# Kernel tuning notes

Measured on AMD Instinct MI355X. Metric: run time of the kernel, lower is better.

Reference implementation:

```python
import jax, jax.numpy as jnp
import numpy as np

N_NODES = 100000
N_EDGES = 1600000
N_GRAPHS = 5000
IN_DIM = 14   # 11 QM9 node features + 3 pos coords
HID = 256


def setup_inputs() -> dict:
    key = jax.random.key(0)
    ks = jax.random.split(key, 12)
    x = jax.random.normal(ks[0], (N_NODES, 11), dtype=jnp.float32)
    pos = jax.random.normal(ks[1], (N_NODES, 3), dtype=jnp.float32)
    edge_index = jax.random.randint(ks[2], (2, N_EDGES), 0, N_NODES, dtype=jnp.int32)
    batch = jnp.sort(jax.random.randint(ks[3], (N_NODES,), 0, N_GRAPHS, dtype=jnp.int32))
    # SAGEConv params (PyG default: lin_l on mean-aggregated neighbors w/ bias, lin_r on root no bias)
    s1 = 1.0 / np.sqrt(IN_DIM)
    s2 = 1.0 / np.sqrt(HID)
    W1l = jax.random.uniform(ks[4], (IN_DIM, HID), jnp.float32, -s1, s1)
    b1 = jax.random.uniform(ks[5], (HID,), jnp.float32, -s1, s1)
    W1r = jax.random.uniform(ks[6], (IN_DIM, HID), jnp.float32, -s1, s1)
    W2l = jax.random.uniform(ks[7], (HID, HID), jnp.float32, -s2, s2)
    b2 = jax.random.uniform(ks[8], (HID,), jnp.float32, -s2, s2)
    W2r = jax.random.uniform(ks[9], (HID, HID), jnp.float32, -s2, s2)
    Wout = jax.random.uniform(ks[10], (HID, 1), jnp.float32, -s2, s2)
    bout = jax.random.uniform(ks[11], (1,), jnp.float32, -s2, s2)
    return {"x": x, "pos": pos, "edge_index": edge_index, "batch": batch,
            "W1l": W1l, "b1": b1, "W1r": W1r,
            "W2l": W2l, "b2": b2, "W2r": W2r,
            "Wout": Wout, "bout": bout}


def _sage_conv(h, src, dst, Wl, bl, Wr):
    # mean aggregation of source node features into destination nodes
    msg = h[src]                                              # [E, D]
    agg = jax.ops.segment_sum(msg, dst, num_segments=N_NODES)  # [N, D]
    cnt = jax.ops.segment_sum(jnp.ones((src.shape[0],), h.dtype), dst,
                              num_segments=N_NODES)
    mean = agg / jnp.maximum(cnt, 1.0)[:, None]
    return mean @ Wl + bl + h @ Wr


def reference(x, pos, edge_index, batch, W1l, b1, W1r, W2l, b2, W2r, Wout, bout):
    src, dst = edge_index[0], edge_index[1]
    h = jnp.concatenate([x, pos], axis=1)                     # [N, 14]
    h = jax.nn.relu(_sage_conv(h, src, dst, W1l, b1, W1r))    # [N, HID]
    h = jax.nn.relu(_sage_conv(h, src, dst, W2l, b2, W2r))    # [N, HID]
    # global mean pool over graphs
    gsum = jax.ops.segment_sum(h, batch, num_segments=N_GRAPHS)  # [G, HID]
    gcnt = jax.ops.segment_sum(jnp.ones((h.shape[0],), h.dtype), batch,
                               num_segments=N_GRAPHS)
    g = gsum / jnp.maximum(gcnt, 1.0)[:, None]
    return g @ Wout + bout                                    # [G, 1]
```

## Files before the change

### kernel.cpp

```cpp
#include <hip/hip_runtime.h>

#define N_N 100000
#define N_E 1600000
#define N_G 5000
#define HID 256
#define IND 14

#define NBUK 391
#define CAP 5120
#define CH3 8192
#define NFB 196

typedef __bf16 bf16x8 __attribute__((ext_vector_type(8)));
typedef float f32x4 __attribute__((ext_vector_type(4)));
typedef unsigned short u16;
typedef unsigned int u32;

constexpr size_t OFF_OUTS  = 0;
constexpr size_t OFF_GCUR  = 5120;
constexpr size_t ZERO_END  = 11520;
constexpr size_t ZERO_BYTES = ZERO_END * 4;
constexpr size_t OFF_GCNT  = 11520;
constexpr size_t OFF_ROWP  = 16640;
constexpr size_t OFF_DEG   = 116736;
constexpr size_t OFF_EBUF  = 216832;
constexpr size_t OFF_CSRC  = 2218752;
constexpr size_t OFF_H1B   = 4220672;
constexpr size_t OFF_WCAT  = 17032960;
constexpr size_t OFF_XP    = 17098496;
constexpr size_t OFF_MEAN1B= 17898496;
constexpr size_t OFF_W1CAT = 30710784;

__device__ __forceinline__ u32 f2b(float f) {
    u32 u = __float_as_uint(f);
    u32 r = u + 0x7FFFu + ((u >> 16) & 1u);
    return r >> 16;
}

#define ADD8(acc, v) do { \
    acc[0] += __uint_as_float(v.x << 16); \
    acc[1] += __uint_as_float(v.x & 0xFFFF0000u); \
    acc[2] += __uint_as_float(v.y << 16); \
    acc[3] += __uint_as_float(v.y & 0xFFFF0000u); \
    acc[4] += __uint_as_float(v.z << 16); \
    acc[5] += __uint_as_float(v.z & 0xFFFF0000u); \
    acc[6] += __uint_as_float(v.w << 16); \
    acc[7] += __uint_as_float(v.w & 0xFFFF0000u); \
} while (0)

#define PACK_N (N_N * 16)
#define WCAT_N (256 * 512)
#define W1CAT_N (256 * 32)
#define PREP_TOT (PACK_N + WCAT_N + W1CAT_N + N_G)
#define PREP_BLKS ((PREP_TOT + 511) / 512)
__global__ __launch_bounds__(512) void k_bfill_prep(const int* __restrict__ ei, int* __restrict__ gcur,
                                                    u32* __restrict__ ebuf,
                                                    const float* __restrict__ x, const float* __restrict__ pos,
                                                    const int* __restrict__ batch,
                                                    const float* __restrict__ W2l, const float* __restrict__ W2r,
                                                    const float* __restrict__ W1l, const float* __restrict__ W1r,
                                                    u16* __restrict__ xpb, float* __restrict__ gcnt,
                                                    u16* __restrict__ wcat, u16* __restrict__ w1cat) {
    __shared__ int hist[NBUK];
    __shared__ int lcur[NBUK];
    __shared__ int gbase[NBUK];
    __shared__ int wsum[8];
    __shared__ u32 stage[CH3];
    __shared__ u16 bstage[CH3];
    int t = threadIdx.x;
    if (blockIdx.x >= NFB) {
        int idx = (blockIdx.x - NFB) * 512 + t;
        if (idx < PACK_N) {
            int n = idx >> 4, f = idx & 15;
            float v = 0.f;
            if (f < 11) v = x[n * 11 + f];
            else if (f < 14) v = pos[n * 3 + (f - 11)];
            xpb[idx] = (u16)f2b(v);
        } else if (idx < PACK_N + WCAT_N) {
            int i2 = idx - PACK_N;
            int n = i2 >> 9, k = i2 & 511;
            float v = (k < 256) ? W2l[k * HID + n] : W2r[(k - 256) * HID + n];
            wcat[(size_t)n * 512 + k] = (u16)f2b(v);
        } else if (idx < PACK_N + WCAT_N + W1CAT_N) {
            int i2 = idx - PACK_N - WCAT_N;
            int n = i2 >> 5, k = i2 & 31;
            float v = 0.f;
            if (k < IND) v = W1l[k * HID + n];
            else if (k >= 16 && k < 16 + IND) v = W1r[(k - 16) * HID + n];
            w1cat[(size_t)n * 32 + k] = (u16)f2b(v);
        } else if (idx < PREP_TOT) {
            int g = idx - PACK_N - WCAT_N - W1CAT_N;
            int lo = 0, hi = N_N;
            while (lo < hi) { int mid = (lo + hi) >> 1; if (batch[mid] < g) lo = mid + 1; else hi = mid; }
            int lo2 = lo, hi2 = N_N;
            while (lo2 < hi2) { int mid = (lo2 + hi2) >> 1; if (batch[mid] < g + 1) lo2 = mid + 1; else hi2 = mid; }
            gcnt[g] = (float)(lo2 - lo);
        }
        return;
    }
    int lane = t & 63, wv = t >> 6;
    int base = blockIdx.x * CH3;
    for (int i = t; i < NBUK; i += 512) hist[i] = 0;
    __syncthreads();
#pragma unroll
    for (int i = 0; i < 16; i++) {
        int e = base + i * 512 + t;
        if (e < N_E) atomicAdd(&hist[ei[N_E + e] >> 8], 1);
    }
    __syncthreads();
    int v = (t < NBUK) ? hist[t] : 0;
    int inc = v;
#pragma unroll
    for (int off = 1; off < 64; off <<= 1) {
        int u = __shfl_up(inc, off, 64);
        if (lane >= off) inc += u;
    }
    if (lane == 63) wsum[wv] = inc;
    __syncthreads();
    int pre = 0;
    for (int i = 0; i < wv; i++) pre += wsum[i];
    int inclusive = inc + pre;
    int excl = inclusive - v;
    if (t < NBUK) lcur[t] = excl;
    int blockcnt = 0;
#pragma unroll
    for (int i = 0; i < 8; i++) blockcnt += wsum[i];
    __syncthreads();
#pragma unroll
    for (int i = 0; i < 16; i++) {
        int e = base + i * 512 + t;
        if (e < N_E) {
            int d = ei[N_E + e];
            int s = ei[e];
            int b = d >> 8;
            int p = atomicAdd(&lcur[b], 1);
            stage[p] = (u32)s | ((u32)(d & 255) << 17);
            bstage[p] = (u16)b;
        }
    }
    __syncthreads();
    if (t < NBUK) {
        int c = hist[t];
        int o = c ? atomicAdd(&gcur[t * 16], c) : 0;
        gbase[t] = t * CAP + o - excl;
    }
    __syncthreads();
#pragma unroll
    for (int i = 0; i < 16; i++) {
        int p = i * 512 + t;
        if (p < blockcnt) {
            int b = bstage[p];
            ebuf[gbase[b] + p] = stage[p];
        }
    }
}

__global__ __launch_bounds__(256) void k_sort(const u32* __restrict__ ebuf, const int* __restrict__ gcur,
                                              int* __restrict__ csrc, int* __restrict__ deg,
                                              int* __restrict__ rowp) {
    __shared__ int degL[256];
    __shared__ int curL[256];
    __shared__ int wsum[4];
    int t = threadIdx.x;
    int lane = t & 63, wv = t >> 6;
    int b = blockIdx.x;
    int bs = b * CAP;
    int be = bs + gcur[b * 16];
    degL[t] = 0;
    __syncthreads();
    for (int e = bs + t; e < be; e += 256)
        atomicAdd(&degL[ebuf[e] >> 17], 1);
    __syncthreads();
    int myDeg = degL[t];
    int inc = myDeg;
#pragma unroll
    for (int off = 1; off < 64; off <<= 1) {
        int u = __shfl_up(inc, off, 64);
        if (lane >= off) inc += u;
    }
    if (lane == 63) wsum[wv] = inc;
    __syncthreads();
    int pre = 0;
    for (int i = 0; i < wv; i++) pre += wsum[i];
    int excl = inc + pre - myDeg;
    int node = (b << 8) + t;
    deg[node] = myDeg;
    rowp[node] = bs + excl;
    curL[t] = bs + excl;
    __syncthreads();
    for (int e = bs + t; e < be; e += 256) {
        u32 w = ebuf[e];
        int p = atomicAdd(&curL[w >> 17], 1);
        csrc[p] = (int)(w & 0x1FFFFu);
    }
}

__global__ __launch_bounds__(256) void k_layer1(const u16* __restrict__ xpb,
                                                const int* __restrict__ rowp, const int* __restrict__ deg,
                                                const int* __restrict__ csrc,
                                                const u16* __restrict__ w1cat, const float* __restrict__ b1,
                                                u16* __restrict__ h1b) {
    __shared__ u16 As[16][32];
    __shared__ u16 outS[16][256];
    int tid = threadIdx.x;
    int wave = tid >> 6, lane = tid & 63;
    int fp = lane & 7;
    int eg = lane >> 3;
#pragma unroll
    for (int nn = 0; nn < 4; nn++) {
        int s = wave * 4 + nn;
        int node = blockIdx.x * 16 + s;
        int st = rowp[node], dg = deg[node];
        int end = st + dg;
        float a0 = 0.f, a1 = 0.f, b0 = 0.f, b1v = 0.f;
        int e = st + eg;
        for (; e + 8 < end; e += 16) {
            int nb1 = csrc[e];
            int nb2 = csrc[e + 8];
            u32 v1 = *(const u32*)(xpb + (size_t)nb1 * 16 + fp * 2);
            u32 v2 = *(const u32*)(xpb + (size_t)nb2 * 16 + fp * 2);
            a0 += __uint_as_float(v1 << 16);
            a1 += __uint_as_float(v1 & 0xFFFF0000u);
            b0 += __uint_as_float(v2 << 16);
            b1v += __uint_as_float(v2 & 0xFFFF0000u);
        }
        if (e < end) {
            int nb = csrc[e];
            u32 v = *(const u32*)(xpb + (size_t)nb * 16 + fp * 2);
            a0 += __uint_as_float(v << 16);
            a1 += __uint_as_float(v & 0xFFFF0000u);
        }
        a0 += b0; a1 += b1v;
        if (eg == 1) {
            *(u32*)&As[s][16 + fp * 2] = *(const u32*)(xpb + (size_t)node * 16 + fp * 2);
        }
#pragma unroll
        for (int off = 32; off >= 8; off >>= 1) {
            a0 += __shfl_down(a0, off);
            a1 += __shfl_down(a1, off);
        }
        if (eg == 0) {
            float inv = 1.f / (float)max(dg, 1);
            *(u32*)&As[s][fp * 2] = f2b(a0 * inv) | (f2b(a1 * inv) << 16);
        }
    }
    __syncthreads();
    int quad = lane >> 4, m16 = lane & 15;
    bf16x8 afrag = *(const bf16x8*)&As[m16][quad * 8];
#pragma unroll
    for (int u = 0; u < 4; u++) {
        int feat = wave * 64 + u * 16 + m16;
        bf16x8 bfrag = *(const bf16x8*)(w1cat + (size_t)feat * 32 + quad * 8);
        f32x4 d = {0.f, 0.f, 0.f, 0.f};
        d = __builtin_amdgcn_mfma_f32_16x16x32_bf16(afrag, bfrag, d, 0, 0, 0);
        float bj = b1[feat];
#pragma unroll
        for (int i = 0; i < 4; i++) {
            int row = quad * 4 + i;
            outS[row][feat] = (u16)f2b(fmaxf(d[i] + bj, 0.f));
        }
    }
    __syncthreads();
    int r = tid >> 4, c = tid & 15;
    uint4* dst = (uint4*)(h1b + ((size_t)(blockIdx.x * 16 + r)) * HID + c * 16);
    dst[0] = *(const uint4*)&outS[r][c * 16];
    dst[1] = *(const uint4*)&outS[r][c * 16 + 8];
}

__global__ __launch_bounds__(256) void k_agg(const u16* __restrict__ h1b, const int* __restrict__ rowp,
                                             const int* __restrict__ deg, const int* __restrict__ csrc,
                                             u16* __restrict__ mean1b) {
    int tid = threadIdx.x;
    int node = blockIdx.x * 4 + (tid >> 6);
    int lane = tid & 63;
    int half = lane >> 5, l32 = lane & 31;
    int st = rowp[node], dg = deg[node];
    int end = st + dg;
    const size_t roff = (size_t)l32 * 8;
    float accA[8] = {}, accB[8] = {};
    int e = st + half;
    for (; e + 2 < end; e += 4) {
        int nb1 = csrc[e];
        int nb2 = csrc[e + 2];
        uint4 v1 = *(const uint4*)(h1b + (size_t)nb1 * HID + roff);
        uint4 v2 = *(const uint4*)(h1b + (size_t)nb2 * HID + roff);
        ADD8(accA, v1);
        ADD8(accB, v2);
    }
    if (e < end) {
        int nb = csrc[e];
        uint4 v = *(const uint4*)(h1b + (size_t)nb * HID + roff);
        ADD8(accA, v);
    }
    float acc[8];
#pragma unroll
    for (int j = 0; j < 8; j++) acc[j] = accA[j] + accB[j];
#pragma unroll
    for (int j = 0; j < 8; j++) acc[j] += __shfl_down(acc[j], 32);
    if (lane < 32) {
        float inv = 1.f / (float)max(dg, 1);
        uint4 o;
        o.x = f2b(acc[0] * inv) | (f2b(acc[1] * inv) << 16);
        o.y = f2b(acc[2] * inv) | (f2b(acc[3] * inv) << 16);
        o.z = f2b(acc[4] * inv) | (f2b(acc[5] * inv) << 16);
        o.w = f2b(acc[6] * inv) | (f2b(acc[7] * inv) << 16);
        *(uint4*)(mean1b + (size_t)node * HID + roff) = o;
    }
}

__global__ __launch_bounds__(256, 2) void k_layer2(const u16* __restrict__ mean1b, const u16* __restrict__ h1b,
                                                   const u16* __restrict__ wcat, const float* __restrict__ b2,
                                                   const int* __restrict__ batch, const float* __restrict__ Wout,
                                                   float* __restrict__ outsum) {
    __shared__ u16 Bs[2][256][40];
    int tid = threadIdx.x;
    int wave = tid >> 6, lane = tid & 63;
    int quad = lane >> 4, m16 = lane & 15;
    int bm = blockIdx.x;
    const size_t r0 = (size_t)(bm * 128 + wave * 32 + m16) * HID + quad * 8;
    const size_t r1 = r0 + 16 * HID;
    f32x4 acc[2][16] = {};
    uint4 a0 = *(const uint4*)(mean1b + r0);
    uint4 a1 = *(const uint4*)(mean1b + r1);
    for (int kt2 = 0; kt2 < 8; kt2++) {
        __syncthreads();
#pragma unroll
        for (int h = 0; h < 2; h++) {
            int kt = kt2 * 2 + h;
#pragma unroll
            for (int i = 0; i < 4; i++) {
                int cidx = tid + 256 * i;
                int n = cidx >> 2, kc = cidx & 3;
                *(uint4*)&Bs[h][n][kc * 8] =
                    *(const uint4*)(wcat + (size_t)n * 512 + kt * 32 + kc * 8);
            }
        }
        __syncthreads();
#pragma unroll
        for (int h = 0; h < 2; h++) {
            int kt = kt2 * 2 + h;
            uint4 cur0 = a0, cur1 = a1;
            if (kt < 15) {
                int kg = (kt + 1) * 32;
                const u16* An = (kg < 256) ? (mean1b + kg) : (h1b + (kg - 256));
                a0 = *(const uint4*)(An + r0);
                a1 = *(const uint4*)(An + r1);
            }
            bf16x8 af0 = __builtin_bit_cast(bf16x8, cur0);
            bf16x8 af1 = __builtin_bit_cast(bf16x8, cur1);
#pragma unroll
            for (int u = 0; u < 16; u++) {
                bf16x8 bf = *(const bf16x8*)&Bs[h][u * 16 + m16][quad * 8];
                acc[0][u] = __builtin_amdgcn_mfma_f32_16x16x32_bf16(af0, bf, acc[0][u], 0, 0, 0);
                acc[1][u] = __builtin_amdgcn_mfma_f32_16x16x32_bf16(af1, bf, acc[1][u], 0, 0, 0);
            }
        }
    }
    float wo[16], bb[16];
#pragma unroll
    for (int u = 0; u < 16; u++) { int col = u * 16 + m16; wo[u] = Wout[col]; bb[u] = b2[col]; }
#pragma unroll
    for (int t = 0; t < 2; t++) {
#pragma unroll
        for (int i = 0; i < 4; i++) {
            float p = 0.f;
#pragma unroll
            for (int u = 0; u < 16; u++)
                p = fmaf(fmaxf(acc[t][u][i] + bb[u], 0.f), wo[u], p);
#pragma unroll
            for (int off = 8; off > 0; off >>= 1) p += __shfl_down(p, off, 16);
            int row = bm * 128 + wave * 32 + t * 16 + quad * 4 + i;
            if (m16 == 0 && row < N_N) atomicAdd(&outsum[batch[row]], p);
        }
    }
}

__global__ __launch_bounds__(256) void k_out(const float* __restrict__ outsum, const float* __restrict__ gcnt,
                                             const float* __restrict__ bout, float* __restrict__ out) {
    int g = blockIdx.x * 256 + threadIdx.x;
    if (g < N_G) out[g] = outsum[g] / fmaxf(gcnt[g], 1.f) + bout[0];
}

extern "C" void kernel_launch(void* const* d_in, const int* in_sizes, int n_in,
                              void* d_out, int out_size, void* d_ws, size_t ws_size,
                              hipStream_t stream) {
    const float* x    = (const float*)d_in[0];
    const float* pos  = (const float*)d_in[1];
    const int*   ei   = (const int*)d_in[2];
    const int*   batch= (const int*)d_in[3];
    const float* W1l  = (const float*)d_in[4];
    const float* b1   = (const float*)d_in[5];
    const float* W1r  = (const float*)d_in[6];
    const float* W2l  = (const float*)d_in[7];
    const float* b2   = (const float*)d_in[8];
    const float* W2r  = (const float*)d_in[9];
    const float* Wout = (const float*)d_in[10];
    const float* bout = (const float*)d_in[11];
    float* out = (float*)d_out;
    float* ws  = (float*)d_ws;

    float* outs  = ws + OFF_OUTS;
    int*   gcur  = (int*)(ws + OFF_GCUR);
    float* gcnt  = ws + OFF_GCNT;
    int*   rowp  = (int*)(ws + OFF_ROWP);
    int*   deg   = (int*)(ws + OFF_DEG);
    u32*   ebuf  = (u32*)(ws + OFF_EBUF);
    int*   csrc  = (int*)(ws + OFF_CSRC);
    u16*   h1b   = (u16*)(ws + OFF_H1B);
    u16*   wcat  = (u16*)(ws + OFF_WCAT);
    u16*   xpb   = (u16*)(ws + OFF_XP);
    u16*   mean1b= (u16*)(ws + OFF_MEAN1B);
    u16*   w1cat = (u16*)(ws + OFF_W1CAT);

    hipMemsetAsync(d_ws, 0, ZERO_BYTES, stream);
    k_bfill_prep<<<NFB + PREP_BLKS, 512, 0, stream>>>(
        ei, gcur, ebuf, x, pos, batch, W2l, W2r, W1l, W1r, xpb, gcnt, wcat, w1cat);
    k_sort  <<<NBUK, 256, 0, stream>>>(ebuf, gcur, csrc, deg, rowp);
    k_layer1<<<N_N / 16, 256, 0, stream>>>(xpb, rowp, deg, csrc, w1cat, b1, h1b);
    k_agg   <<<N_N / 4, 256, 0, stream>>>(h1b, rowp, deg, csrc, mean1b);
    k_layer2<<<(N_N + 127) / 128, 256, 0, stream>>>(mean1b, h1b, wcat, b2, batch, Wout, outs);
    k_out   <<<(N_G + 255) / 256, 256, 0, stream>>>(outs, gcnt, bout, out);
}
```

Measured before the change: 325.0 us.

## Recompute layer-1 outputs per edge from compact 32-wide inputs instead of gathering h1

Layer 1 now also writes each node's 32-wide bf16 input row (mean-aggregated features plus root features) into a scratch buffer that reuses the edge buffer. The second aggregation no longer gathers 256-wide h1 rows per neighbor. It gathers the 32-wide rows and recomputes relu(z·W1+b1) per edge with MFMA, masking padded lanes, then averages. This replaces 512-byte gathers with 64-byte gathers at the cost of redundant matrix math per edge, about 16 MFMAs per 16 edges per wave.

```diff
diff --git a/kernel.cpp b/kernel.cpp
--- a/kernel.cpp
+++ b/kernel.cpp
@@ -199,7 +199,7 @@
                                                 const int* __restrict__ rowp, const int* __restrict__ deg,
                                                 const int* __restrict__ csrc,
                                                 const u16* __restrict__ w1cat, const float* __restrict__ b1,
-                                                u16* __restrict__ h1b) {
+                                                u16* __restrict__ h1b, u16* __restrict__ zb) {
     __shared__ u16 As[16][32];
     __shared__ u16 outS[16][256];
     int tid = threadIdx.x;
@@ -245,6 +245,10 @@
         }
     }
     __syncthreads();
+    {
+        int s = tid >> 4, kp = tid & 15;
+        *(u32*)(zb + (size_t)(blockIdx.x * 16 + s) * 32 + kp * 2) = *(const u32*)&As[s][kp * 2];
+    }
     int quad = lane >> 4, m16 = lane & 15;
     bf16x8 afrag = *(const bf16x8*)&As[m16][quad * 8];
 #pragma unroll
@@ -267,45 +271,53 @@
     dst[1] = *(const uint4*)&outS[r][c * 16 + 8];
 }
 
-__global__ __launch_bounds__(256) void k_agg(const u16* __restrict__ h1b, const int* __restrict__ rowp,
+__global__ __launch_bounds__(256) void k_agg(const u16* __restrict__ zb, const int* __restrict__ rowp,
                                              const int* __restrict__ deg, const int* __restrict__ csrc,
+                                             const u16* __restrict__ w1cat, const float* __restrict__ b1,
                                              u16* __restrict__ mean1b) {
+    __shared__ u16 outW[4][256];
     int tid = threadIdx.x;
-    int node = blockIdx.x * 4 + (tid >> 6);
-    int lane = tid & 63;
-    int half = lane >> 5, l32 = lane & 31;
+    int wv = tid >> 6, lane = tid & 63;
+    int quad = lane >> 4, m16 = lane & 15;
+    int node = blockIdx.x * 4 + wv;
     int st = rowp[node], dg = deg[node];
     int end = st + dg;
-    const size_t roff = (size_t)l32 * 8;
-    float accA[8] = {}, accB[8] = {};
-    int e = st + half;
-    for (; e + 2 < end; e += 4) {
-        int nb1 = csrc[e];
-        int nb2 = csrc[e + 2];
-        uint4 v1 = *(const uint4*)(h1b + (size_t)nb1 * HID + roff);
-        uint4 v2 = *(const uint4*)(h1b + (size_t)nb2 * HID + roff);
-        ADD8(accA, v1);
-        ADD8(accB, v2);
-    }
-    if (e < end) {
-        int nb = csrc[e];
-        uint4 v = *(const uint4*)(h1b + (size_t)nb * HID + roff);
-        ADD8(accA, v);
-    }
-    float acc[8];
-#pragma unroll
-    for (int j = 0; j < 8; j++) acc[j] = accA[j] + accB[j];
-#pragma unroll
-    for (int j = 0; j < 8; j++) acc[j] += __shfl_down(acc[j], 32);
-    if (lane < 32) {
-        float inv = 1.f / (float)max(dg, 1);
-        uint4 o;
-        o.x = f2b(acc[0] * inv) | (f2b(acc[1] * inv) << 16);
-        o.y = f2b(acc[2] * inv) | (f2b(acc[3] * inv) << 16);
-        o.z = f2b(acc[4] * inv) | (f2b(acc[5] * inv) << 16);
-        o.w = f2b(acc[6] * inv) | (f2b(acc[7] * inv) << 16);
-        *(uint4*)(mean1b + (size_t)node * HID + roff) = o;
-    }
+
+    bf16x8 bfrag[16];
+    float bb[16];
+#pragma unroll
+    for (int u = 0; u < 16; u++) {
+        bfrag[u] = *(const bf16x8*)(w1cat + (size_t)(u * 16 + m16) * 32 + quad * 8);
+        bb[u] = b1[u * 16 + m16];
+    }
+    float acc[16] = {};
+    for (int cb = 0; cb < dg; cb += 16) {
+        int e = st + cb + m16;
+        int nb = (e < end) ? csrc[e] : csrc[st];
+        bf16x8 afrag = *(const bf16x8*)(zb + (size_t)nb * 32 + quad * 8);
+        float mk[4];
+#pragma unroll
+        for (int i = 0; i < 4; i++)
+            mk[i] = (cb + quad * 4 + i < dg) ? 1.f : 0.f;
+#pragma unroll
+        for (int u = 0; u < 16; u++) {
+            f32x4 d = {0.f, 0.f, 0.f, 0.f};
+            d = __builtin_amdgcn_mfma_f32_16x16x32_bf16(afrag, bfrag[u], d, 0, 0, 0);
+#pragma unroll
+            for (int i = 0; i < 4; i++)
+                acc[u] = fmaf(mk[i], fmaxf(d[i] + bb[u], 0.f), acc[u]);
+        }
+    }
+    float inv = 1.f / (float)max(dg, 1);
+#pragma unroll
+    for (int u = 0; u < 16; u++) {
+        float a = acc[u];
+        a += __shfl_down(a, 32);
+        a += __shfl_down(a, 16);
+        if (quad == 0) outW[wv][u * 16 + m16] = (u16)f2b(a * inv);
+    }
+    if (lane < 32)
+        *(uint4*)(mean1b + (size_t)node * HID + (size_t)lane * 8) = *(const uint4*)&outW[wv][lane * 8];
 }
 
 __global__ __launch_bounds__(256, 2) void k_layer2(const u16* __restrict__ mean1b, const u16* __restrict__ h1b,
@@ -411,13 +423,14 @@
     u16*   xpb   = (u16*)(ws + OFF_XP);
     u16*   mean1b= (u16*)(ws + OFF_MEAN1B);
     u16*   w1cat = (u16*)(ws + OFF_W1CAT);
+    u16*   zb    = (u16*)ebuf;
 
     hipMemsetAsync(d_ws, 0, ZERO_BYTES, stream);
     k_bfill_prep<<<NFB + PREP_BLKS, 512, 0, stream>>>(
         ei, gcur, ebuf, x, pos, batch, W2l, W2r, W1l, W1r, xpb, gcnt, wcat, w1cat);
     k_sort  <<<NBUK, 256, 0, stream>>>(ebuf, gcur, csrc, deg, rowp);
-    k_layer1<<<N_N / 16, 256, 0, stream>>>(xpb, rowp, deg, csrc, w1cat, b1, h1b);
-    k_agg   <<<N_N / 4, 256, 0, stream>>>(h1b, rowp, deg, csrc, mean1b);
+    k_layer1<<<N_N / 16, 256, 0, stream>>>(xpb, rowp, deg, csrc, w1cat, b1, h1b, zb);
+    k_agg   <<<N_N / 4, 256, 0, stream>>>(zb, rowp, deg, csrc, w1cat, b1, mean1b);
     k_layer2<<<(N_N + 127) / 128, 256, 0, stream>>>(mean1b, h1b, wcat, b2, batch, Wout, outs);
     k_out   <<<(N_G + 255) / 256, 256, 0, stream>>>(outs, gcnt, bout, out);
 }
```

Result: slower. 659.7 us (+103.0%).

## Split neighbor aggregation into feature-slice passes for cache locality

Applied to the files above, without the earlier changes.

Restructures the mean-aggregation kernel so the grid is split into 16 passes, each covering a 16-feature slice of every node. Each node is handled by two threads, one per 8-feature half, and the cross-lane shuffle reduction is removed. Each pass's gather working set (a 32-byte slice per node) is small enough to stay cache-resident, which is meant to cut random-gather traffic to HBM. The cost is that the CSR index arrays are re-read in every pass, each thread issues narrow 16-byte scattered loads, and padding to 782×128 nodes means the last block reads past the end of the rowp and deg arrays.

```diff
diff --git a/kernel.cpp b/kernel.cpp
--- a/kernel.cpp
+++ b/kernel.cpp
@@ -267,45 +267,45 @@
     dst[1] = *(const uint4*)&outS[r][c * 16 + 8];
 }
 
+#define NPASS 16
+#define AGG_BPP 782
 __global__ __launch_bounds__(256) void k_agg(const u16* __restrict__ h1b, const int* __restrict__ rowp,
                                              const int* __restrict__ deg, const int* __restrict__ csrc,
                                              u16* __restrict__ mean1b) {
     int tid = threadIdx.x;
-    int node = blockIdx.x * 4 + (tid >> 6);
-    int lane = tid & 63;
-    int half = lane >> 5, l32 = lane & 31;
+    int pass = blockIdx.x / AGG_BPP;
+    int blk  = blockIdx.x % AGG_BPP;
+    int node = blk * 128 + (tid >> 1);
+    int fh = tid & 1;
     int st = rowp[node], dg = deg[node];
     int end = st + dg;
-    const size_t roff = (size_t)l32 * 8;
+    const u16* src = h1b + (size_t)pass * 16 + (size_t)fh * 8;
     float accA[8] = {}, accB[8] = {};
-    int e = st + half;
-    for (; e + 2 < end; e += 4) {
+    int e = st;
+    for (; e + 1 < end; e += 2) {
         int nb1 = csrc[e];
-        int nb2 = csrc[e + 2];
-        uint4 v1 = *(const uint4*)(h1b + (size_t)nb1 * HID + roff);
-        uint4 v2 = *(const uint4*)(h1b + (size_t)nb2 * HID + roff);
+        int nb2 = csrc[e + 1];
+        uint4 v1 = *(const uint4*)(src + (size_t)nb1 * HID);
+        uint4 v2 = *(const uint4*)(src + (size_t)nb2 * HID);
         ADD8(accA, v1);
         ADD8(accB, v2);
     }
     if (e < end) {
         int nb = csrc[e];
-        uint4 v = *(const uint4*)(h1b + (size_t)nb * HID + roff);
+        uint4 v = *(const uint4*)(src + (size_t)nb * HID);
         ADD8(accA, v);
     }
-    float acc[8];
-#pragma unroll
-    for (int j = 0; j < 8; j++) acc[j] = accA[j] + accB[j];
-#pragma unroll
-    for (int j = 0; j < 8; j++) acc[j] += __shfl_down(acc[j], 32);
-    if (lane < 32) {
-        float inv = 1.f / (float)max(dg, 1);
-        uint4 o;
-        o.x = f2b(acc[0] * inv) | (f2b(acc[1] * inv) << 16);
-        o.y = f2b(acc[2] * inv) | (f2b(acc[3] * inv) << 16);
-        o.z = f2b(acc[4] * inv) | (f2b(acc[5] * inv) << 16);
-        o.w = f2b(acc[6] * inv) | (f2b(acc[7] * inv) << 16);
-        *(uint4*)(mean1b + (size_t)node * HID + roff) = o;
-    }
+    float inv = 1.f / (float)max(dg, 1);
+    float a0 = (accA[0] + accB[0]) * inv, a1 = (accA[1] + accB[1]) * inv;
+    float a2 = (accA[2] + accB[2]) * inv, a3 = (accA[3] + accB[3]) * inv;
+    float a4 = (accA[4] + accB[4]) * inv, a5 = (accA[5] + accB[5]) * inv;
+    float a6 = (accA[6] + accB[6]) * inv, a7 = (accA[7] + accB[7]) * inv;
+    uint4 o;
+    o.x = f2b(a0) | (f2b(a1) << 16);
+    o.y = f2b(a2) | (f2b(a3) << 16);
+    o.z = f2b(a4) | (f2b(a5) << 16);
+    o.w = f2b(a6) | (f2b(a7) << 16);
+    *(uint4*)(mean1b + (size_t)node * HID + (size_t)pass * 16 + (size_t)fh * 8) = o;
 }
 
 __global__ __launch_bounds__(256, 2) void k_layer2(const u16* __restrict__ mean1b, const u16* __restrict__ h1b,
@@ -417,7 +417,7 @@
         ei, gcur, ebuf, x, pos, batch, W2l, W2r, W1l, W1r, xpb, gcnt, wcat, w1cat);
     k_sort  <<<NBUK, 256, 0, stream>>>(ebuf, gcur, csrc, deg, rowp);
     k_layer1<<<N_N / 16, 256, 0, stream>>>(xpb, rowp, deg, csrc, w1cat, b1, h1b);
-    k_agg   <<<N_N / 4, 256, 0, stream>>>(h1b, rowp, deg, csrc, mean1b);
+    k_agg   <<<AGG_BPP * NPASS, 256, 0, stream>>>(h1b, rowp, deg, csrc, mean1b);
     k_layer2<<<(N_N + 127) / 128, 256, 0, stream>>>(mean1b, h1b, wcat, b2, batch, Wout, outs);
     k_out   <<<(N_G + 255) / 256, 256, 0, stream>>>(outs, gcnt, bout, out);
 }
```

New measurement: 676.0 us. +108.0%, slower.
